# Performance work log

Measured on AMD Instinct MI355X. Metric: run time of the kernel, lower is better.

## Reference

```python
import jax, jax.numpy as jnp
import numpy as np
import math

BLOCK = 256
NUM_HEADS = 32
HEAD_DIM = 128
HIDDEN = 2048
INNER = NUM_HEADS * HEAD_DIM
SEQ = 4096
EPS = 1e-5
LAYER_IDX = 0
NUM_LAYERS = 32


def _build_slopes(n):
    def get_slopes(n):
        def pow2(m):
            start = 2 ** (-2 ** (-(math.log2(m) - 3)))
            return [start * start ** i for i in range(m)]
        if math.log2(n).is_integer():
            return pow2(n)
        c = 2 ** math.floor(math.log2(n))
        return pow2(c) + get_slopes(2 * c)[0::2][: n - c]
    s = np.asarray(get_slopes(n), dtype=np.float32).reshape(n, 1, 1)
    # layer decay scaling as in __init__
    s = s * (1.0 - LAYER_IDX / (NUM_LAYERS - 1) + 1e-5)
    return s


def setup_inputs() -> dict:
    key = jax.random.key(0)
    k1, k2, k3, k4 = jax.random.split(key, 4)
    sd_h = 1.0 / math.sqrt(HIDDEN)
    sd_i = 1.0 / math.sqrt(INNER)
    return {
        "hidden_states": jax.random.normal(k1, (SEQ, HIDDEN), jnp.float32),
        "w_qkv": jax.random.normal(k2, (HIDDEN, 3 * INNER), jnp.float32) * sd_h,
        "w_gate": jax.random.normal(k3, (HIDDEN, INNER), jnp.float32) * sd_h,
        "w_out": jax.random.normal(k4, (INNER, HIDDEN), jnp.float32) * sd_i,
        "norm_weight": jnp.ones((INNER,), jnp.float32),
        "slope_rate": jnp.asarray(_build_slopes(NUM_HEADS)),
        "kv_cache": jnp.zeros((NUM_HEADS, HEAD_DIM, HEAD_DIM), jnp.float32),
    }


def _lightning_attention(q, k, v, slope, kv0):
    # q,k,v: [h, n, d]; slope: [h,1,1]; kv0: [h, d, d]
    h, n, d = q.shape
    nb = n // BLOCK
    qb = q.reshape(h, nb, BLOCK, d).transpose(1, 0, 2, 3)  # [nb,h,B,d]
    kb = k.reshape(h, nb, BLOCK, d).transpose(1, 0, 2, 3)
    vb = v.reshape(h, nb, BLOCK, d).transpose(1, 0, 2, 3)

    idx = jnp.arange(BLOCK, dtype=jnp.float32)
    diff = idx[:, None] - idx[None, :]                      # i - j
    s = slope.reshape(h, 1, 1)
    intra_decay = jnp.where(diff >= 0, jnp.exp(-s * diff), 0.0)   # [h,B,B]
    q_decay = jnp.exp(-s * (idx + 1.0).reshape(1, BLOCK, 1))      # [h,B,1]
    k_decay = jnp.exp(-s * (BLOCK - 1.0 - idx).reshape(1, BLOCK, 1))  # [h,B,1]
    block_decay = jnp.exp(-s * BLOCK)                             # [h,1,1]

    def step(kv, blk):
        qc, kc, vc = blk  # each [h,B,d]
        scores = jnp.einsum('hid,hjd->hij', qc, kc) * intra_decay
        o_intra = jnp.einsum('hij,hjd->hid', scores, vc)
        o_inter = q_decay * jnp.einsum('hid,hde->hie', qc, kv)
        kv_new = block_decay * kv + jnp.einsum('hjd,hje->hde', kc * k_decay, vc)
        return kv_new, o_intra + o_inter

    kv_final, outs = jax.lax.scan(step, kv0, (qb, kb, vb))
    out = outs.transpose(1, 0, 2, 3).reshape(h, n, d)
    return out, kv_final


def reference(hidden_states, w_qkv, w_gate, w_out, norm_weight, slope_rate, kv_cache):
    n = hidden_states.shape[0]
    # qkv projection + SiLU activation (done in fp32 in the original)
    qkv = jax.nn.silu(hidden_states @ w_qkv)                  # [n, 3*inner]
    qkv = qkv.reshape(n, NUM_HEADS, 3 * HEAD_DIM)
    q, k, v = jnp.split(qkv, 3, axis=-1)                      # [n,h,d] each
    q = q.transpose(1, 0, 2)                                  # [h,n,d]
    k = k.transpose(1, 0, 2)
    v = v.transpose(1, 0, 2)

    attn, kv_final = _lightning_attention(q, k, v, slope_rate, kv_cache)
    attn = attn.transpose(1, 0, 2).reshape(n, INNER)          # n (h d)

    # RMSNorm (fp32) then sigmoid gate then output projection
    var = jnp.mean(attn * attn, axis=-1, keepdims=True)
    normed = attn * jax.lax.rsqrt(var + EPS) * norm_weight
    gate = jax.nn.sigmoid(hidden_states @ w_gate)
    out = (gate * normed) @ w_out                             # [n, hidden]
    return out
```

## Files before the change

kernel.cpp:

```cpp
#include <hip/hip_runtime.h>
#include <stdint.h>

typedef __bf16 bf16x8 __attribute__((ext_vector_type(8)));
typedef float  f32x4  __attribute__((ext_vector_type(4)));
typedef unsigned short u16x8 __attribute__((ext_vector_type(8)));

__device__ __forceinline__ unsigned short f2bf(float f) {
    union { float f; uint32_t u; } x; x.f = f;
    uint32_t r = (x.u + 0x7FFFu + ((x.u >> 16) & 1u)) >> 16;
    return (unsigned short)r;
}
__device__ __forceinline__ float bf2f(unsigned short b) {
    union { uint32_t u; float f; } x; x.u = ((uint32_t)b) << 16;
    return x.f;
}

__device__ __forceinline__ void gl16(const void* g, void* l) {
    __builtin_amdgcn_global_load_lds(
        (const __attribute__((address_space(1))) void*)g,
        (__attribute__((address_space(3))) void*)(uint32_t)(uintptr_t)l,
        16, 0, 0);
}

#define MFMA16(a, b, c) __builtin_amdgcn_mfma_f32_16x16x32_bf16((a), (b), (c), 0, 0, 0)

__global__ __launch_bounds__(256) void f32_to_bf16_kernel(const float* __restrict__ in,
                                                          unsigned short* __restrict__ out,
                                                          int n8) {
    int i = blockIdx.x * 256 + threadIdx.x;
    if (i >= n8) return;
    float4 a = ((const float4*)in)[2 * i];
    float4 b = ((const float4*)in)[2 * i + 1];
    u16x8 o;
    o[0] = f2bf(a.x); o[1] = f2bf(a.y); o[2] = f2bf(a.z); o[3] = f2bf(a.w);
    o[4] = f2bf(b.x); o[5] = f2bf(b.y); o[6] = f2bf(b.z); o[7] = f2bf(b.w);
    ((u16x8*)out)[i] = o;
}

__global__ __launch_bounds__(256) void transpose_w_kernel(const float* __restrict__ in,
                                                          unsigned short* __restrict__ out,
                                                          int R, int C) {
    __shared__ float tile[32][33];
    int c0 = blockIdx.x * 32, r0 = blockIdx.y * 32;
    int lx = threadIdx.x & 31, ly = threadIdx.x >> 5;
#pragma unroll
    for (int i = ly; i < 32; i += 8)
        tile[i][lx] = in[(size_t)(r0 + i) * C + c0 + lx];
    __syncthreads();
#pragma unroll
    for (int i = ly; i < 32; i += 8)
        out[(size_t)(c0 + i) * R + r0 + lx] = f2bf(tile[lx][i]);
}

template <int ACT>
__global__ __launch_bounds__(512, 2) void gemm256_kernel(const unsigned short* __restrict__ A,
                                                         const unsigned short* __restrict__ Bt,
                                                         unsigned short* __restrict__ Cout,
                                                         int N, int K, int NBN) {
    __shared__ unsigned short Abuf[2][2][8192];
    __shared__ unsigned short Bbuf[2][2][8192];

    int nwg = gridDim.x;
    int bid = blockIdx.x;
    int wg = (bid & 7) * (nwg >> 3) + (bid >> 3);
    int bm = wg / NBN, bn = wg % NBN;
    int tid = threadIdx.x, lane = tid & 63, w = tid >> 6;
    int wr = w >> 2, wc = w & 3;

    int r0 = tid >> 3;
    int cbs = (tid & 7) << 4;
    int el0 = (cbs ^ ((r0 & 7) << 4)) >> 1;
    int r1 = 64 + r0;
    int el1 = (cbs ^ ((r1 & 7) << 4)) >> 1;
    int lo0 = tid * 16, lo1 = 8192 + tid * 16;

    const unsigned short* Ag0 = A + (size_t)(bm * 256) * K;
    const unsigned short* Ag1 = A + (size_t)(bm * 256 + 128) * K;
    const unsigned short* Bg0 = Bt + (size_t)(bn * 256) * K;
    const unsigned short* Bg1 = Bt + (size_t)(bn * 256 + 128) * K;

#define STAGE(src, dstHalf, k0)                                   \
    do {                                                          \
        gl16((src) + (size_t)r0 * K + (k0) + el0, (char*)(dstHalf) + lo0); \
        gl16((src) + (size_t)r1 * K + (k0) + el1, (char*)(dstHalf) + lo1); \
    } while (0)

    int aRow = wr * 64 + (lane & 15);
    int bRow = wc * 32 + (lane & 15);
    int swz = (lane & 7) << 4;
    int cbb = (lane >> 4) << 4;

#define RD_A(cur, R, m, kk) \
    af[R][m][kk] = *(const bf16x8*)((const char*)Abuf[cur][R] + ((aRow + (m) * 16) << 7) + (((kk) * 64 + cbb) ^ swz))
#define RD_B(cur, Cq, n, kk) \
    bfr[n][kk] = *(const bf16x8*)((const char*)Bbuf[cur][Cq] + ((bRow + (n) * 16) << 7) + (((kk) * 64 + cbb) ^ swz))

    bf16x8 af[2][4][2];
    bf16x8 bfr[2][2];
    f32x4 acc[4][4][2];
#pragma unroll
    for (int q = 0; q < 4; ++q)
#pragma unroll
        for (int m = 0; m < 4; ++m)
#pragma unroll
            for (int n = 0; n < 2; ++n)
#pragma unroll
                for (int r = 0; r < 4; ++r) acc[q][m][n][r] = 0.f;

    int NT = K >> 6;
    STAGE(Ag0, Abuf[0][0], 0);
    STAGE(Bg0, Bbuf[0][0], 0);
    STAGE(Ag1, Abuf[0][1], 0);
    STAGE(Bg1, Bbuf[0][1], 0);
    asm volatile("s_waitcnt vmcnt(4)" ::: "memory");
    __builtin_amdgcn_s_barrier();

    for (int t = 0; t < NT; ++t) {
        int cur = t & 1, nx = cur ^ 1;
        int kn = (t + 1) << 6;
        bool ds = (t + 1 < NT);

#pragma unroll
        for (int m = 0; m < 4; ++m) { RD_A(cur, 0, m, 0); RD_A(cur, 0, m, 1); }
#pragma unroll
        for (int n = 0; n < 2; ++n) { RD_B(cur, 0, n, 0); RD_B(cur, 0, n, 1); }
        if (ds) STAGE(Ag0, Abuf[nx][0], kn);
        asm volatile("s_waitcnt lgkmcnt(8)" ::: "memory");
        __builtin_amdgcn_s_barrier();
        asm volatile("s_waitcnt lgkmcnt(0)" ::: "memory");
        __builtin_amdgcn_sched_barrier(0);
        __builtin_amdgcn_s_setprio(1);
#pragma unroll
        for (int m = 0; m < 4; ++m)
#pragma unroll
            for (int n = 0; n < 2; ++n) {
                acc[0][m][n] = MFMA16(af[0][m][0], bfr[n][0], acc[0][m][n]);
                acc[0][m][n] = MFMA16(af[0][m][1], bfr[n][1], acc[0][m][n]);
            }
        __builtin_amdgcn_s_setprio(0);
        asm volatile("s_waitcnt vmcnt(4)" ::: "memory");
        __builtin_amdgcn_s_barrier();

#pragma unroll
        for (int m = 0; m < 4; ++m) { RD_A(cur, 1, m, 0); RD_A(cur, 1, m, 1); }
        if (ds) STAGE(Bg0, Bbuf[nx][0], kn);
        __builtin_amdgcn_s_barrier();
        asm volatile("s_waitcnt lgkmcnt(0)" ::: "memory");
        __builtin_amdgcn_sched_barrier(0);
        __builtin_amdgcn_s_setprio(1);
#pragma unroll
        for (int m = 0; m < 4; ++m)
#pragma unroll
            for (int n = 0; n < 2; ++n) {
                acc[1][m][n] = MFMA16(af[1][m][0], bfr[n][0], acc[1][m][n]);
                acc[1][m][n] = MFMA16(af[1][m][1], bfr[n][1], acc[1][m][n]);
            }
        __builtin_amdgcn_s_setprio(0);
        asm volatile("s_waitcnt vmcnt(4)" ::: "memory");
        __builtin_amdgcn_s_barrier();

#pragma unroll
        for (int n = 0; n < 2; ++n) { RD_B(cur, 1, n, 0); RD_B(cur, 1, n, 1); }
        if (ds) STAGE(Ag1, Abuf[nx][1], kn);
        __builtin_amdgcn_s_barrier();
        asm volatile("s_waitcnt lgkmcnt(0)" ::: "memory");
        __builtin_amdgcn_sched_barrier(0);
        __builtin_amdgcn_s_setprio(1);
#pragma unroll
        for (int m = 0; m < 4; ++m)
#pragma unroll
            for (int n = 0; n < 2; ++n) {
                acc[2][m][n] = MFMA16(af[0][m][0], bfr[n][0], acc[2][m][n]);
                acc[2][m][n] = MFMA16(af[0][m][1], bfr[n][1], acc[2][m][n]);
            }
        __builtin_amdgcn_s_setprio(0);
        __builtin_amdgcn_s_barrier();

        if (ds) STAGE(Bg1, Bbuf[nx][1], kn);
        __builtin_amdgcn_s_barrier();
        __builtin_amdgcn_s_setprio(1);
#pragma unroll
        for (int m = 0; m < 4; ++m)
#pragma unroll
            for (int n = 0; n < 2; ++n) {
                acc[3][m][n] = MFMA16(af[1][m][0], bfr[n][0], acc[3][m][n]);
                acc[3][m][n] = MFMA16(af[1][m][1], bfr[n][1], acc[3][m][n]);
            }
        __builtin_amdgcn_s_setprio(0);
        asm volatile("s_waitcnt vmcnt(4)" ::: "memory");
        __builtin_amdgcn_s_barrier();
    }

#pragma unroll
    for (int q = 0; q < 4; ++q) {
        const int R_ = q & 1, C_ = q >> 1;
#pragma unroll
        for (int m = 0; m < 4; ++m) {
            int row0 = bm * 256 + R_ * 128 + wr * 64 + m * 16 + ((lane >> 4) * 4);
#pragma unroll
            for (int n = 0; n < 2; ++n) {
                int col = bn * 256 + C_ * 128 + wc * 32 + n * 16 + (lane & 15);
#pragma unroll
                for (int rg = 0; rg < 4; ++rg) {
                    float v = acc[q][m][n][rg];
                    if (ACT == 1) v = v / (1.f + __expf(-v));
                    else if (ACT == 2) v = 1.f / (1.f + __expf(-v));
                    Cout[(size_t)(row0 + rg) * N + col] = f2bf(v);
                }
            }
        }
    }
#undef STAGE
#undef RD_A
#undef RD_B
}

template <int ACT, int OUTBF>
__global__ __launch_bounds__(256) void gemm_bt_kernel(const unsigned short* __restrict__ A,
                                                      const unsigned short* __restrict__ Bt,
                                                      void* __restrict__ Cp,
                                                      int M, int N, int K) {
    __shared__ unsigned short As[128 * 64];
    __shared__ unsigned short Bs[128 * 64];
    int bn = blockIdx.x, bm = blockIdx.y;
    int tid = threadIdx.x, lane = tid & 63, w = tid >> 6;
    int wr = w >> 1, wc = w & 1;

    f32x4 acc[4][4];
#pragma unroll
    for (int m = 0; m < 4; ++m)
#pragma unroll
        for (int n = 0; n < 4; ++n)
#pragma unroll
            for (int r = 0; r < 4; ++r) acc[m][n][r] = 0.f;

    const size_t Abase = (size_t)bm * 128 * K;
    const size_t Bbase = (size_t)bn * 128 * K;

    for (int k0 = 0; k0 < K; k0 += 64) {
        __syncthreads();
#pragma unroll
        for (int it = 0; it < 4; ++it) {
            int slot = it * 256 + tid;
            int o = slot * 16;
            int r = o >> 7;
            int cb = o & 127;
            int scb = cb ^ ((r & 7) << 4);
            gl16(A + Abase + (size_t)r * K + k0 + (scb >> 1), (char*)As + o);
            gl16(Bt + Bbase + (size_t)r * K + k0 + (scb >> 1), (char*)Bs + o);
        }
        __syncthreads();
#pragma unroll
        for (int kk = 0; kk < 2; ++kk) {
            int kb = kk * 64 + ((lane >> 4) * 16);
            bf16x8 af[4], bfr[4];
#pragma unroll
            for (int m = 0; m < 4; ++m) {
                int r = wr * 64 + m * 16 + (lane & 15);
                af[m] = *(const bf16x8*)((const char*)As + (r << 7) + (kb ^ ((r & 7) << 4)));
            }
#pragma unroll
            for (int n = 0; n < 4; ++n) {
                int r = wc * 64 + n * 16 + (lane & 15);
                bfr[n] = *(const bf16x8*)((const char*)Bs + (r << 7) + (kb ^ ((r & 7) << 4)));
            }
#pragma unroll
            for (int m = 0; m < 4; ++m)
#pragma unroll
                for (int n = 0; n < 4; ++n)
                    acc[m][n] = MFMA16(af[m], bfr[n], acc[m][n]);
        }
    }

#pragma unroll
    for (int m = 0; m < 4; ++m) {
        int rowb = bm * 128 + wr * 64 + m * 16 + ((lane >> 4) * 4);
#pragma unroll
        for (int n = 0; n < 4; ++n) {
            int col = bn * 128 + wc * 64 + n * 16 + (lane & 15);
#pragma unroll
            for (int r = 0; r < 4; ++r) {
                float v = acc[m][n][r];
                if (ACT == 1) v = v / (1.f + __expf(-v));
                else if (ACT == 2) v = 1.f / (1.f + __expf(-v));
                size_t idx = (size_t)(rowb + r) * N + col;
                if (OUTBF) ((unsigned short*)Cp)[idx] = f2bf(v);
                else       ((float*)Cp)[idx] = v;
            }
        }
    }
}

__global__ __launch_bounds__(256) void kv_transpose_kernel(const unsigned short* __restrict__ qkv,
                                                           const float* __restrict__ slopes,
                                                           unsigned short* __restrict__ kts,
                                                           unsigned short* __restrict__ vt) {
    __shared__ unsigned short tk[32][33];
    __shared__ unsigned short tv[32][33];
    int n0 = blockIdx.x * 32, d0 = blockIdx.y * 32, h = blockIdx.z;
    float s = slopes[h];
    int lx = threadIdx.x & 31, ly = threadIdx.x >> 5;
#pragma unroll
    for (int i = ly; i < 32; i += 8) {
        int n = n0 + i;
        size_t rowb = (size_t)n * 12288 + h * 384;
        float kv = bf2f(qkv[rowb + 128 + d0 + lx]) * __expf(-s * (float)(255 - (n & 255)));
        tk[i][lx] = f2bf(kv);
        tv[i][lx] = qkv[rowb + 256 + d0 + lx];
    }
    __syncthreads();
#pragma unroll
    for (int i = ly; i < 32; i += 8) {
        size_t ob = (size_t)(h * 128 + d0 + i) * 4096 + n0 + lx;
        kts[ob] = tk[lx][i];
        vt[ob] = tv[lx][i];
    }
}

__global__ __launch_bounds__(256) void kv_outer_kernel(const unsigned short* __restrict__ kts,
                                                       const unsigned short* __restrict__ vt,
                                                       float* __restrict__ U) {
    __shared__ unsigned short Kc[128 * 64];
    __shared__ unsigned short Vc[128 * 64];
    int blk = blockIdx.x;
    int h = blk & 31, t = blk >> 5;
    int tid = threadIdx.x, lane = tid & 63, w = tid >> 6;

    f32x4 acc[2][8];
#pragma unroll
    for (int m = 0; m < 2; ++m)
#pragma unroll
        for (int n = 0; n < 8; ++n)
#pragma unroll
            for (int r = 0; r < 4; ++r) acc[m][n][r] = 0.f;

    for (int ks = 0; ks < 4; ++ks) {
        __syncthreads();
#pragma unroll
        for (int it = 0; it < 4; ++it) {
            int slot = it * 256 + tid;
            int o = slot * 16;
            int r = o >> 7;
            int cb = o & 127;
            int scb = cb ^ ((r & 7) << 4);
            size_t j = (size_t)t * 256 + ks * 64 + (scb >> 1);
            gl16(kts + (size_t)(h * 128 + r) * 4096 + j, (char*)Kc + o);
            gl16(vt + (size_t)(h * 128 + r) * 4096 + j, (char*)Vc + o);
        }
        __syncthreads();
#pragma unroll
        for (int kk = 0; kk < 2; ++kk) {
            int kb = kk * 64 + ((lane >> 4) * 16);
            bf16x8 vf[2], kf[8];
#pragma unroll
            for (int m = 0; m < 2; ++m) {
                int e = w * 32 + m * 16 + (lane & 15);
                vf[m] = *(const bf16x8*)((const char*)Vc + (e << 7) + (kb ^ ((e & 7) << 4)));
            }
#pragma unroll
            for (int n = 0; n < 8; ++n) {
                int d = n * 16 + (lane & 15);
                kf[n] = *(const bf16x8*)((const char*)Kc + (d << 7) + (kb ^ ((d & 7) << 4)));
            }
#pragma unroll
            for (int m = 0; m < 2; ++m)
#pragma unroll
                for (int n = 0; n < 8; ++n)
                    acc[m][n] = MFMA16(vf[m], kf[n], acc[m][n]);
        }
    }
    size_t base = (size_t)(h * 16 + t) * 16384;
#pragma unroll
    for (int m = 0; m < 2; ++m)
#pragma unroll
        for (int n = 0; n < 8; ++n)
#pragma unroll
            for (int r = 0; r < 4; ++r) {
                int e = w * 32 + m * 16 + ((lane >> 4) * 4) + r;
                int d = n * 16 + (lane & 15);
                U[base + (size_t)e * 128 + d] = acc[m][n][r];
            }
}

__global__ __launch_bounds__(256) void kv_scan_kernel(const float* __restrict__ kv_cache,
                                                      const float* __restrict__ U,
                                                      const float* __restrict__ slopes,
                                                      unsigned short* __restrict__ Wb) {
    int h = blockIdx.x >> 3;
    int c0 = (blockIdx.x & 7) * 2048;
    int tid = threadIdx.x;
    float s = slopes[h];
    float bd = __expf(-s * 256.f);
    float wst[8];
    size_t hb = (size_t)h * 16384;
#pragma unroll
    for (int i = 0; i < 8; ++i) {
        int idx = c0 + i * 256 + tid;
        int e = idx >> 7, d = idx & 127;
        wst[i] = kv_cache[hb + (size_t)d * 128 + e];
    }
    for (int t = 0; t < 16; ++t) {
        size_t base = (size_t)(h * 16 + t) * 16384 + c0;
#pragma unroll
        for (int i = 0; i < 8; ++i) {
            int idx = i * 256 + tid;
            Wb[base + idx] = f2bf(wst[i]);
            wst[i] = bd * wst[i] + U[base + idx];
        }
    }
}

__global__ __launch_bounds__(256, 1) void attn_out_kernel(const unsigned short* __restrict__ qkv,
                                                          const unsigned short* __restrict__ vt,
                                                          const unsigned short* __restrict__ Wb,
                                                          const float* __restrict__ slopes,
                                                          unsigned short* __restrict__ attn) {
    __shared__ unsigned short lds[65536];
    unsigned short* Qs = lds;
    unsigned short* Ps = lds + 32768;
    unsigned short* KW = lds + 49152;
    unsigned short* Ks = KW;
    unsigned short* Vs = KW + 8192;

    int blk = blockIdx.x;
    int h = blk & 31, t = blk >> 5;
    float s = slopes[h];
    int tid = threadIdx.x, lane = tid & 63, w = tid >> 6;

#pragma unroll
    for (int it = 0; it < 16; ++it) {
        int slot = it * 256 + tid;
        int o = slot * 16;
        int r = o >> 8, cb = o & 255, scb = cb ^ ((r & 7) << 4);
        gl16(qkv + (size_t)(t * 256 + r) * 12288 + h * 384 + (scb >> 1), (char*)Qs + o);
    }
#pragma unroll
    for (int it = 0; it < 8; ++it) {
        int slot = it * 256 + tid;
        int o = slot * 16;
        int e = o >> 8, cb = o & 255, scb = cb ^ ((e & 7) << 4);
        gl16(Wb + (size_t)((h * 16 + t) * 128 + e) * 128 + (scb >> 1), (char*)KW + o);
    }
    __syncthreads();

    f32x4 acc[4][8];
#pragma unroll
    for (int m = 0; m < 4; ++m)
#pragma unroll
        for (int n = 0; n < 8; ++n)
#pragma unroll
            for (int r = 0; r < 4; ++r) acc[m][n][r] = 0.f;

#pragma unroll
    for (int kk = 0; kk < 4; ++kk) {
        int kb = kk * 64 + ((lane >> 4) * 16);
        bf16x8 qf[4], wf[8];
#pragma unroll
        for (int m = 0; m < 4; ++m) {
            int r = w * 64 + m * 16 + (lane & 15);
            qf[m] = *(const bf16x8*)((const char*)Qs + (r << 8) + (kb ^ ((r & 7) << 4)));
        }
#pragma unroll
        for (int n = 0; n < 8; ++n) {
            int e = n * 16 + (lane & 15);
            wf[n] = *(const bf16x8*)((const char*)KW + (e << 8) + (kb ^ ((e & 7) << 4)));
        }
#pragma unroll
        for (int m = 0; m < 4; ++m)
#pragma unroll
            for (int n = 0; n < 8; ++n)
                acc[m][n] = MFMA16(qf[m], wf[n], acc[m][n]);
    }
#pragma unroll
    for (int m = 0; m < 4; ++m)
#pragma unroll
        for (int rg = 0; rg < 4; ++rg) {
            int i = w * 64 + m * 16 + ((lane >> 4) * 4) + rg;
            float qd = __expf(-s * (float)(i + 1));
#pragma unroll
            for (int n = 0; n < 8; ++n) acc[m][n][rg] *= qd;
        }

    for (int jb = 0; jb < 4; ++jb) {
        __syncthreads();
#pragma unroll
        for (int it = 0; it < 4; ++it) {
            int slot = it * 256 + tid;
            int o = slot * 16;
            int r = o >> 8, cb = o & 255, scb = cb ^ ((r & 7) << 4);
            gl16(qkv + (size_t)(t * 256 + jb * 64 + r) * 12288 + h * 384 + 128 + (scb >> 1),
                 (char*)Ks + o);
        }
#pragma unroll
        for (int it = 0; it < 4; ++it) {
            int slot = it * 256 + tid;
            int o = slot * 16;
            int e = o >> 7, cb = o & 127, scb = cb ^ ((e & 7) << 4);
            gl16(vt + (size_t)(h * 128 + e) * 4096 + t * 256 + jb * 64 + (scb >> 1),
                 (char*)Vs + o);
        }
        __syncthreads();

        if (jb <= w) {
            f32x4 sc[4][4];
#pragma unroll
            for (int m = 0; m < 4; ++m)
#pragma unroll
                for (int n = 0; n < 4; ++n)
#pragma unroll
                    for (int r = 0; r < 4; ++r) sc[m][n][r] = 0.f;
#pragma unroll
            for (int kk = 0; kk < 4; ++kk) {
                int kb = kk * 64 + ((lane >> 4) * 16);
                bf16x8 qf[4], kf[4];
#pragma unroll
                for (int m = 0; m < 4; ++m) {
                    int r = w * 64 + m * 16 + (lane & 15);
                    qf[m] = *(const bf16x8*)((const char*)Qs + (r << 8) + (kb ^ ((r & 7) << 4)));
                }
#pragma unroll
                for (int n = 0; n < 4; ++n) {
                    int r = n * 16 + (lane & 15);
                    kf[n] = *(const bf16x8*)((const char*)Ks + (r << 8) + (kb ^ ((r & 7) << 4)));
                }
#pragma unroll
                for (int m = 0; m < 4; ++m)
#pragma unroll
                    for (int n = 0; n < 4; ++n)
                        sc[m][n] = MFMA16(qf[m], kf[n], sc[m][n]);
            }
            unsigned short* Pw = Ps + w * 4096;
#pragma unroll
            for (int m = 0; m < 4; ++m)
#pragma unroll
                for (int n = 0; n < 4; ++n)
#pragma unroll
                    for (int rg = 0; rg < 4; ++rg) {
                        int il = m * 16 + ((lane >> 4) * 4) + rg;
                        int i = w * 64 + il;
                        int jl = n * 16 + (lane & 15);
                        int j = jb * 64 + jl;
                        float v = 0.f;
                        if (i >= j) v = sc[m][n][rg] * __expf(-s * (float)(i - j));
                        int cb2 = (jl * 2) ^ ((il & 7) << 4);
                        *(unsigned short*)((char*)Pw + (il << 7) + cb2) = f2bf(v);
                    }
            asm volatile("s_waitcnt lgkmcnt(0)" ::: "memory");
#pragma unroll
            for (int kk = 0; kk < 2; ++kk) {
                int kb = kk * 64 + ((lane >> 4) * 16);
                bf16x8 pf[4], vf[8];
#pragma unroll
                for (int m = 0; m < 4; ++m) {
                    int il = m * 16 + (lane & 15);
                    pf[m] = *(const bf16x8*)((const char*)Pw + (il << 7) + (kb ^ ((il & 7) << 4)));
                }
#pragma unroll
                for (int n = 0; n < 8; ++n) {
                    int e = n * 16 + (lane & 15);
                    vf[n] = *(const bf16x8*)((const char*)Vs + (e << 7) + (kb ^ ((e & 7) << 4)));
                }
#pragma unroll
                for (int m = 0; m < 4; ++m)
#pragma unroll
                    for (int n = 0; n < 8; ++n)
                        acc[m][n] = MFMA16(pf[m], vf[n], acc[m][n]);
            }
        }
    }

#pragma unroll
    for (int m = 0; m < 4; ++m)
#pragma unroll
        for (int n = 0; n < 8; ++n)
#pragma unroll
            for (int rg = 0; rg < 4; ++rg) {
                int i = w * 64 + m * 16 + ((lane >> 4) * 4) + rg;
                int col = h * 128 + n * 16 + (lane & 15);
                attn[(size_t)(t * 256 + i) * 4096 + col] = f2bf(acc[m][n][rg]);
            }
}

__global__ __launch_bounds__(256) void rms_gate_kernel(const unsigned short* __restrict__ attn,
                                                       const unsigned short* __restrict__ gate,
                                                       const float* __restrict__ nw,
                                                       unsigned short* __restrict__ gated) {
    int row = blockIdx.x, tid = threadIdx.x;
    int lane = tid & 63, w = tid >> 6;
    const unsigned short* ar = attn + (size_t)row * 4096 + tid * 16;
    u16x8 a0 = *(const u16x8*)ar;
    u16x8 a1 = *(const u16x8*)(ar + 8);
    float v[16];
    float ss = 0.f;
#pragma unroll
    for (int j = 0; j < 8; ++j) { v[j] = bf2f(a0[j]); v[8 + j] = bf2f(a1[j]); }
#pragma unroll
    for (int j = 0; j < 16; ++j) ss += v[j] * v[j];
#pragma unroll
    for (int o = 32; o > 0; o >>= 1) ss += __shfl_xor(ss, o);
    __shared__ float red[4];
    if (lane == 0) red[w] = ss;
    __syncthreads();
    float tot = red[0] + red[1] + red[2] + red[3];
    float rs = rsqrtf(tot * (1.f / 4096.f) + 1e-5f);
    const unsigned short* gr = gate + (size_t)row * 4096 + tid * 16;
    u16x8 g0 = *(const u16x8*)gr;
    u16x8 g1 = *(const u16x8*)(gr + 8);
    const float* nwp = nw + tid * 16;
    u16x8 o0, o1;
#pragma unroll
    for (int j = 0; j < 8; ++j) {
        o0[j] = f2bf(v[j] * rs * nwp[j] * bf2f(g0[j]));
        o1[j] = f2bf(v[8 + j] * rs * nwp[8 + j] * bf2f(g1[j]));
    }
    unsigned short* gp = gated + (size_t)row * 4096 + tid * 16;
    *(u16x8*)gp = o0;
    *(u16x8*)(gp + 8) = o1;
}

extern "C" void kernel_launch(void* const* d_in, const int* in_sizes, int n_in,
                              void* d_out, int out_size, void* d_ws, size_t ws_size,
                              hipStream_t stream) {
    const float* hs       = (const float*)d_in[0];
    const float* w_qkv    = (const float*)d_in[1];
    const float* w_gate   = (const float*)d_in[2];
    const float* w_out    = (const float*)d_in[3];
    const float* nw       = (const float*)d_in[4];
    const float* slopes   = (const float*)d_in[5];
    const float* kv_cache = (const float*)d_in[6];
    float* out = (float*)d_out;
    char* ws = (char*)d_ws;

    unsigned short* hsb  = (unsigned short*)(ws + 0);
    unsigned short* wqt  = (unsigned short*)(ws + 16777216);
    unsigned short* wgt  = (unsigned short*)(ws + 67108864);
    unsigned short* wot  = (unsigned short*)(ws + 83886080);
    unsigned short* qkv  = (unsigned short*)(ws + 100663296);
    unsigned short* gate = (unsigned short*)(ws + 201326592);
    unsigned short* kts  = (unsigned short*)(ws + 234881024);
    unsigned short* vt   = (unsigned short*)(ws + 268435456);
    float*          U    = (float*)(ws + 301989888);
    unsigned short* Wb   = (unsigned short*)(ws + 335544320);
    unsigned short* attn  = wqt;
    unsigned short* gated = qkv;

    f32_to_bf16_kernel<<<4096, 256, 0, stream>>>(hs, hsb, 1048576);
    {
        dim3 g(384, 64);
        transpose_w_kernel<<<g, 256, 0, stream>>>(w_qkv, wqt, 2048, 12288);
    }
    {
        dim3 g(128, 64);
        transpose_w_kernel<<<g, 256, 0, stream>>>(w_gate, wgt, 2048, 4096);
    }
    {
        dim3 g(64, 128);
        transpose_w_kernel<<<g, 256, 0, stream>>>(w_out, wot, 4096, 2048);
    }
    gemm256_kernel<1><<<768, 512, 0, stream>>>(hsb, wqt, qkv, 12288, 2048, 48);
    gemm256_kernel<2><<<256, 512, 0, stream>>>(hsb, wgt, gate, 4096, 2048, 16);
    {
        dim3 g(128, 4, 32);
        kv_transpose_kernel<<<g, 256, 0, stream>>>(qkv, slopes, kts, vt);
    }
    kv_outer_kernel<<<512, 256, 0, stream>>>(kts, vt, U);
    kv_scan_kernel<<<256, 256, 0, stream>>>(kv_cache, U, slopes, Wb);
    attn_out_kernel<<<512, 256, 0, stream>>>(qkv, vt, Wb, slopes, attn);
    rms_gate_kernel<<<4096, 256, 0, stream>>>(attn, gate, nw, gated);
    {
        dim3 g(16, 32);
        gemm_bt_kernel<0, 0><<<g, 256, 0, stream>>>(gated, wot, out, 4096, 2048, 4096);
    }
}
```

Baseline: 575.0 us.

## Deepen gemm256 prefetch pipeline and use it for output projection

Restructures the 256x256 GEMM main loop to prefetch two K-tiles ahead. It issues the next tile's LDS fragment reads during the current tile's MFMA quadrants and keeps B fragments per column half, which cuts barriers per iteration from about six to one. The kernel gains an fp32 output mode, so the final output projection now uses gemm256 (128 workgroups) instead of the simpler 128x128 gemm_bt kernel, which is removed. This adds register pressure from the extra fragment buffers, and with only 128 workgroups the output GEMM may underfill the device.

```diff
diff --git a/kernel.cpp b/kernel.cpp
--- a/kernel.cpp
+++ b/kernel.cpp
@@ -52,10 +52,10 @@
         out[(size_t)(c0 + i) * R + r0 + lx] = f2bf(tile[lx][i]);
 }
 
-template <int ACT>
+template <int ACT, int OUTF32>
 __global__ __launch_bounds__(512, 2) void gemm256_kernel(const unsigned short* __restrict__ A,
                                                          const unsigned short* __restrict__ Bt,
-                                                         unsigned short* __restrict__ Cout,
+                                                         void* __restrict__ Cout,
                                                          int N, int K, int NBN) {
     __shared__ unsigned short Abuf[2][2][8192];
     __shared__ unsigned short Bbuf[2][2][8192];
@@ -79,8 +79,8 @@
     const unsigned short* Bg0 = Bt + (size_t)(bn * 256) * K;
     const unsigned short* Bg1 = Bt + (size_t)(bn * 256 + 128) * K;
 
-#define STAGE(src, dstHalf, k0)                                   \
-    do {                                                          \
+#define STAGE(src, dstHalf, k0)                                            \
+    do {                                                                   \
         gl16((src) + (size_t)r0 * K + (k0) + el0, (char*)(dstHalf) + lo0); \
         gl16((src) + (size_t)r1 * K + (k0) + el1, (char*)(dstHalf) + lo1); \
     } while (0)
@@ -90,13 +90,24 @@
     int swz = (lane & 7) << 4;
     int cbb = (lane >> 4) << 4;
 
-#define RD_A(cur, R, m, kk) \
-    af[R][m][kk] = *(const bf16x8*)((const char*)Abuf[cur][R] + ((aRow + (m) * 16) << 7) + (((kk) * 64 + cbb) ^ swz))
-#define RD_B(cur, Cq, n, kk) \
-    bfr[n][kk] = *(const bf16x8*)((const char*)Bbuf[cur][Cq] + ((bRow + (n) * 16) << 7) + (((kk) * 64 + cbb) ^ swz))
+#define RD_A(slot, R, m, kk) \
+    af[R][m][kk] = *(const bf16x8*)((const char*)Abuf[slot][R] + ((aRow + (m) * 16) << 7) + (((kk) * 64 + cbb) ^ swz))
+#define RD_B(slot, Cq, n, kk) \
+    bfr[Cq][n][kk] = *(const bf16x8*)((const char*)Bbuf[slot][Cq] + ((bRow + (n) * 16) << 7) + (((kk) * 64 + cbb) ^ swz))
+
+#define QUAD(q, Rh, Cc)                                                       \
+    do {                                                                      \
+        _Pragma("unroll")                                                     \
+        for (int m = 0; m < 4; ++m)                                           \
+            _Pragma("unroll")                                                 \
+            for (int n = 0; n < 2; ++n) {                                     \
+                acc[q][m][n] = MFMA16(af[Rh][m][0], bfr[Cc][n][0], acc[q][m][n]); \
+                acc[q][m][n] = MFMA16(af[Rh][m][1], bfr[Cc][n][1], acc[q][m][n]); \
+            }                                                                 \
+    } while (0)
 
     bf16x8 af[2][4][2];
-    bf16x8 bfr[2][2];
+    bf16x8 bfr[2][2][2];
     f32x4 acc[4][4][2];
 #pragma unroll
     for (int q = 0; q < 4; ++q)
@@ -112,83 +123,65 @@
     STAGE(Bg0, Bbuf[0][0], 0);
     STAGE(Ag1, Abuf[0][1], 0);
     STAGE(Bg1, Bbuf[0][1], 0);
-    asm volatile("s_waitcnt vmcnt(4)" ::: "memory");
+    STAGE(Ag0, Abuf[1][0], 64);
+    STAGE(Bg0, Bbuf[1][0], 64);
+    STAGE(Ag1, Abuf[1][1], 64);
+    STAGE(Bg1, Bbuf[1][1], 64);
+    asm volatile("s_waitcnt vmcnt(8)" ::: "memory");
     __builtin_amdgcn_s_barrier();
+#pragma unroll
+    for (int m = 0; m < 4; ++m) { RD_A(0, 0, m, 0); RD_A(0, 0, m, 1); }
+#pragma unroll
+    for (int n = 0; n < 2; ++n) { RD_B(0, 0, n, 0); RD_B(0, 0, n, 1); }
 
     for (int t = 0; t < NT; ++t) {
         int cur = t & 1, nx = cur ^ 1;
-        int kn = (t + 1) << 6;
-        bool ds = (t + 1 < NT);
-
-#pragma unroll
-        for (int m = 0; m < 4; ++m) { RD_A(cur, 0, m, 0); RD_A(cur, 0, m, 1); }
-#pragma unroll
-        for (int n = 0; n < 2; ++n) { RD_B(cur, 0, n, 0); RD_B(cur, 0, n, 1); }
-        if (ds) STAGE(Ag0, Abuf[nx][0], kn);
+        bool rd = (t + 1 < NT);
+        bool st = (t + 2 < NT);
+        int ks = (t + 2) << 6;
+
+#pragma unroll
+        for (int m = 0; m < 4; ++m) { RD_A(cur, 1, m, 0); RD_A(cur, 1, m, 1); }
         asm volatile("s_waitcnt lgkmcnt(8)" ::: "memory");
-        __builtin_amdgcn_s_barrier();
-        asm volatile("s_waitcnt lgkmcnt(0)" ::: "memory");
         __builtin_amdgcn_sched_barrier(0);
         __builtin_amdgcn_s_setprio(1);
-#pragma unroll
-        for (int m = 0; m < 4; ++m)
-#pragma unroll
-            for (int n = 0; n < 2; ++n) {
-                acc[0][m][n] = MFMA16(af[0][m][0], bfr[n][0], acc[0][m][n]);
-                acc[0][m][n] = MFMA16(af[0][m][1], bfr[n][1], acc[0][m][n]);
-            }
+        QUAD(0, 0, 0);
         __builtin_amdgcn_s_setprio(0);
-        asm volatile("s_waitcnt vmcnt(4)" ::: "memory");
-        __builtin_amdgcn_s_barrier();
-
-#pragma unroll
-        for (int m = 0; m < 4; ++m) { RD_A(cur, 1, m, 0); RD_A(cur, 1, m, 1); }
-        if (ds) STAGE(Bg0, Bbuf[nx][0], kn);
-        __builtin_amdgcn_s_barrier();
-        asm volatile("s_waitcnt lgkmcnt(0)" ::: "memory");
+
+#pragma unroll
+        for (int n = 0; n < 2; ++n) { RD_B(cur, 1, n, 0); RD_B(cur, 1, n, 1); }
+        asm volatile("s_waitcnt lgkmcnt(4)" ::: "memory");
         __builtin_amdgcn_sched_barrier(0);
         __builtin_amdgcn_s_setprio(1);
-#pragma unroll
-        for (int m = 0; m < 4; ++m)
-#pragma unroll
-            for (int n = 0; n < 2; ++n) {
-                acc[1][m][n] = MFMA16(af[1][m][0], bfr[n][0], acc[1][m][n]);
-                acc[1][m][n] = MFMA16(af[1][m][1], bfr[n][1], acc[1][m][n]);
-            }
+        QUAD(1, 1, 0);
         __builtin_amdgcn_s_setprio(0);
-        asm volatile("s_waitcnt vmcnt(4)" ::: "memory");
+
+        asm volatile("s_waitcnt lgkmcnt(0)" ::: "memory");
+        asm volatile("s_waitcnt vmcnt(0)" ::: "memory");
         __builtin_amdgcn_s_barrier();
-
-#pragma unroll
-        for (int n = 0; n < 2; ++n) { RD_B(cur, 1, n, 0); RD_B(cur, 1, n, 1); }
-        if (ds) STAGE(Ag1, Abuf[nx][1], kn);
-        __builtin_amdgcn_s_barrier();
-        asm volatile("s_waitcnt lgkmcnt(0)" ::: "memory");
-        __builtin_amdgcn_sched_barrier(0);
+        if (st) {
+            STAGE(Ag0, Abuf[cur][0], ks);
+            STAGE(Bg0, Bbuf[cur][0], ks);
+        }
+        if (rd) {
+#pragma unroll
+            for (int n = 0; n < 2; ++n) { RD_B(nx, 0, n, 0); RD_B(nx, 0, n, 1); }
+        }
         __builtin_amdgcn_s_setprio(1);
-#pragma unroll
-        for (int m = 0; m < 4; ++m)
-#pragma unroll
-            for (int n = 0; n < 2; ++n) {
-                acc[2][m][n] = MFMA16(af[0][m][0], bfr[n][0], acc[2][m][n]);
-                acc[2][m][n] = MFMA16(af[0][m][1], bfr[n][1], acc[2][m][n]);
-            }
+        QUAD(2, 0, 1);
         __builtin_amdgcn_s_setprio(0);
-        __builtin_amdgcn_s_barrier();
-
-        if (ds) STAGE(Bg1, Bbuf[nx][1], kn);
-        __builtin_amdgcn_s_barrier();
+
+        if (st) {
+            STAGE(Ag1, Abuf[cur][1], ks);
+            STAGE(Bg1, Bbuf[cur][1], ks);
+        }
+        if (rd) {
+#pragma unroll
+            for (int m = 0; m < 4; ++m) { RD_A(nx, 0, m, 0); RD_A(nx, 0, m, 1); }
+        }
         __builtin_amdgcn_s_setprio(1);
-#pragma unroll
-        for (int m = 0; m < 4; ++m)
-#pragma unroll
-            for (int n = 0; n < 2; ++n) {
-                acc[3][m][n] = MFMA16(af[1][m][0], bfr[n][0], acc[3][m][n]);
-                acc[3][m][n] = MFMA16(af[1][m][1], bfr[n][1], acc[3][m][n]);
-            }
+        QUAD(3, 1, 1);
         __builtin_amdgcn_s_setprio(0);
-        asm volatile("s_waitcnt vmcnt(4)" ::: "memory");
-        __builtin_amdgcn_s_barrier();
     }
 
 #pragma unroll
@@ -205,7 +198,9 @@
                     float v = acc[q][m][n][rg];
                     if (ACT == 1) v = v / (1.f + __expf(-v));
                     else if (ACT == 2) v = 1.f / (1.f + __expf(-v));
-                    Cout[(size_t)(row0 + rg) * N + col] = f2bf(v);
+                    size_t idx = (size_t)(row0 + rg) * N + col;
+                    if (OUTF32) ((float*)Cout)[idx] = v;
+                    else        ((unsigned short*)Cout)[idx] = f2bf(v);
                 }
             }
         }
@@ -213,82 +208,7 @@
 #undef STAGE
 #undef RD_A
 #undef RD_B
-}
-
-template <int ACT, int OUTBF>
-__global__ __launch_bounds__(256) void gemm_bt_kernel(const unsigned short* __restrict__ A,
-                                                      const unsigned short* __restrict__ Bt,
-                                                      void* __restrict__ Cp,
-                                                      int M, int N, int K) {
-    __shared__ unsigned short As[128 * 64];
-    __shared__ unsigned short Bs[128 * 64];
-    int bn = blockIdx.x, bm = blockIdx.y;
-    int tid = threadIdx.x, lane = tid & 63, w = tid >> 6;
-    int wr = w >> 1, wc = w & 1;
-
-    f32x4 acc[4][4];
-#pragma unroll
-    for (int m = 0; m < 4; ++m)
-#pragma unroll
-        for (int n = 0; n < 4; ++n)
-#pragma unroll
-            for (int r = 0; r < 4; ++r) acc[m][n][r] = 0.f;
-
-    const size_t Abase = (size_t)bm * 128 * K;
-    const size_t Bbase = (size_t)bn * 128 * K;
-
-    for (int k0 = 0; k0 < K; k0 += 64) {
-        __syncthreads();
-#pragma unroll
-        for (int it = 0; it < 4; ++it) {
-            int slot = it * 256 + tid;
-            int o = slot * 16;
-            int r = o >> 7;
-            int cb = o & 127;
-            int scb = cb ^ ((r & 7) << 4);
-            gl16(A + Abase + (size_t)r * K + k0 + (scb >> 1), (char*)As + o);
-            gl16(Bt + Bbase + (size_t)r * K + k0 + (scb >> 1), (char*)Bs + o);
-        }
-        __syncthreads();
-#pragma unroll
-        for (int kk = 0; kk < 2; ++kk) {
-            int kb = kk * 64 + ((lane >> 4) * 16);
-            bf16x8 af[4], bfr[4];
-#pragma unroll
-            for (int m = 0; m < 4; ++m) {
-                int r = wr * 64 + m * 16 + (lane & 15);
-                af[m] = *(const bf16x8*)((const char*)As + (r << 7) + (kb ^ ((r & 7) << 4)));
-            }
-#pragma unroll
-            for (int n = 0; n < 4; ++n) {
-                int r = wc * 64 + n * 16 + (lane & 15);
-                bfr[n] = *(const bf16x8*)((const char*)Bs + (r << 7) + (kb ^ ((r & 7) << 4)));
-            }
-#pragma unroll
-            for (int m = 0; m < 4; ++m)
-#pragma unroll
-                for (int n = 0; n < 4; ++n)
-                    acc[m][n] = MFMA16(af[m], bfr[n], acc[m][n]);
-        }
-    }
-
-#pragma unroll
-    for (int m = 0; m < 4; ++m) {
-        int rowb = bm * 128 + wr * 64 + m * 16 + ((lane >> 4) * 4);
-#pragma unroll
-        for (int n = 0; n < 4; ++n) {
-            int col = bn * 128 + wc * 64 + n * 16 + (lane & 15);
-#pragma unroll
-            for (int r = 0; r < 4; ++r) {
-                float v = acc[m][n][r];
-                if (ACT == 1) v = v / (1.f + __expf(-v));
-                else if (ACT == 2) v = 1.f / (1.f + __expf(-v));
-                size_t idx = (size_t)(rowb + r) * N + col;
-                if (OUTBF) ((unsigned short*)Cp)[idx] = f2bf(v);
-                else       ((float*)Cp)[idx] = v;
-            }
-        }
-    }
+#undef QUAD
 }
 
 __global__ __launch_bounds__(256) void kv_transpose_kernel(const unsigned short* __restrict__ qkv,
@@ -657,8 +577,8 @@
         dim3 g(64, 128);
         transpose_w_kernel<<<g, 256, 0, stream>>>(w_out, wot, 4096, 2048);
     }
-    gemm256_kernel<1><<<768, 512, 0, stream>>>(hsb, wqt, qkv, 12288, 2048, 48);
-    gemm256_kernel<2><<<256, 512, 0, stream>>>(hsb, wgt, gate, 4096, 2048, 16);
+    gemm256_kernel<1, 0><<<768, 512, 0, stream>>>(hsb, wqt, qkv, 12288, 2048, 48);
+    gemm256_kernel<2, 0><<<256, 512, 0, stream>>>(hsb, wgt, gate, 4096, 2048, 16);
     {
         dim3 g(128, 4, 32);
         kv_transpose_kernel<<<g, 256, 0, stream>>>(qkv, slopes, kts, vt);
@@ -667,8 +587,5 @@
     kv_scan_kernel<<<256, 256, 0, stream>>>(kv_cache, U, slopes, Wb);
     attn_out_kernel<<<512, 256, 0, stream>>>(qkv, vt, Wb, slopes, attn);
     rms_gate_kernel<<<4096, 256, 0, stream>>>(attn, gate, nw, gated);
-    {
-        dim3 g(16, 32);
-        gemm_bt_kernel<0, 0><<<g, 256, 0, stream>>>(gated, wot, out, 4096, 2048, 4096);
-    }
-}
+    gemm256_kernel<0, 1><<<128, 512, 0, stream>>>(gated, wot, out, 2048, 4096, 8);
+}
```

Result: no change. 567.1 us (-1.4%).
